# Kernel tuning notes

Hardware: AMD Instinct MI355X
Metric: run time of the kernel (lower is better)

The kernel has to match this reference:

```python
import jax, jax.numpy as jnp
import numpy as np
from jax import lax

N = 50000      # total nodes
E = 400000     # total edges
F = 512        # input feature dim
B = 50         # graphs in batch
NP = 1000      # nodes per graph
OUT = 10       # out_channel
EPS = 1e-5


def setup_inputs():
    key = jax.random.key(0)
    ks = jax.random.split(key, 20)
    x = jax.random.normal(ks[0], (N, F), jnp.float32)
    eg = jnp.arange(E) // (E // B)                       # graph id per edge
    src = jax.random.randint(ks[1], (E,), 0, NP) + eg * NP
    dst = jax.random.randint(ks[2], (E,), 0, NP) + eg * NP
    edge_index = jnp.stack([src, dst]).astype(jnp.int32)
    batch = (jnp.arange(N) // NP).astype(jnp.int32)
    s = 0.02
    W1 = s * jax.random.normal(ks[3], (1024, F), jnp.float32)
    b1 = jnp.zeros((1024,), jnp.float32)
    g1 = jnp.ones((1024,), jnp.float32)
    be1 = jnp.zeros((1024,), jnp.float32)
    Wp = s * jax.random.normal(ks[4], (1, 2 * 1024), jnp.float32)  # EdgePooling lin
    bp = jnp.zeros((1,), jnp.float32)
    W2 = s * jax.random.normal(ks[5], (512, 1024), jnp.float32)
    b2 = jnp.zeros((512,), jnp.float32)
    g2 = jnp.ones((512,), jnp.float32)
    be2 = jnp.zeros((512,), jnp.float32)
    Wfc = s * jax.random.normal(ks[6], (200, 512), jnp.float32)
    bfc = jnp.zeros((200,), jnp.float32)
    Wfc1 = s * jax.random.normal(ks[7], (OUT, 200), jnp.float32)
    bfc1 = jnp.zeros((OUT,), jnp.float32)
    return dict(x=x, edge_index=edge_index, batch=batch, W1=W1, b1=b1, g1=g1,
                be1=be1, Wp=Wp, bp=bp, W2=W2, b2=b2, g2=g2, be2=be2,
                Wfc=Wfc, bfc=bfc, Wfc1=Wfc1, bfc1=bfc1)


def _bn(h, g, b):
    m = h.mean(0)
    v = jnp.var(h, axis=0)  # biased var, as torch BatchNorm1d (train mode)
    return (h - m) * (g / jnp.sqrt(v + EPS)) + b


def _edge_pool(h, src, dst, batch, Wp, bp):
    # raw edge score: Linear([h_src || h_dst]) -> scalar per edge
    e = jnp.concatenate([h[src], h[dst]], axis=-1) @ Wp.T + bp  # [E,1]
    e = e[:, 0]
    # softmax over edges sharing the same destination node (PyG default)
    m = jax.ops.segment_max(e, dst, num_segments=N)
    ex = jnp.exp(e - m[dst])
    den = jax.ops.segment_sum(ex, dst, num_segments=N)
    score = ex / den[dst] + 0.5  # add_to_edge_score = 0.5

    # greedy contraction in descending-score order (sequential, like PyG)
    order = jnp.argsort(-score)
    so, do = src[order], dst[order]

    def step(merged, sd):
        s_, d_ = sd
        ok = (~merged[s_]) & (~merged[d_])
        merged = merged.at[s_].set(merged[s_] | ok)
        merged = merged.at[d_].set(merged[d_] | ok)
        return merged, ok

    _, valid = lax.scan(step, jnp.zeros(N, bool), (so, do))
    ec = (jnp.cumsum(valid.astype(jnp.int32)) - 1)      # cluster id per contracted edge
    num_merged = valid.astype(jnp.int32).sum()

    OOB = jnp.int32(N)
    cluster = jnp.full((N,), -1, jnp.int32)
    cluster = cluster.at[jnp.where(valid, so, OOB)].set(ec, mode='drop')
    cluster = cluster.at[jnp.where(valid, do, OOB)].set(ec, mode='drop')
    unmerged = cluster < 0
    rank = jnp.cumsum(unmerged.astype(jnp.int32)) - 1
    cluster = jnp.where(unmerged, num_merged + rank, cluster)

    # per-cluster multiplier: contracted-edge score, 1.0 for singleton nodes
    mult = jnp.ones((N,), h.dtype)
    mult = mult.at[jnp.where(valid, ec, OOB)].set(score[order], mode='drop')

    new_x = jax.ops.segment_sum(h, cluster, num_segments=N) * mult[:, None]
    new_batch = jnp.full((N,), B, jnp.int32).at[cluster].set(batch)  # pad slots -> dummy graph B
    return new_x, new_batch


def reference(x, edge_index, batch, W1, b1, g1, be1, Wp, bp, W2, b2, g2, be2,
              Wfc, bfc, Wfc1, bfc1):
    src, dst = edge_index[0], edge_index[1]
    # ChebConv K=1 == plain linear (only T_0 = x term)
    h = jax.nn.relu(_bn(x @ W1.T + b1, g1, be1))         # [N,1024]
    h, nb = _edge_pool(h, src, dst, batch, Wp, bp)       # [N,1024] padded, [N]
    h = jax.nn.relu(_bn(h @ W2.T + b2, g2, be2))         # [N,512]
    # global mean pool over graphs (dummy segment B holds padding)
    sums = jax.ops.segment_sum(h, nb, num_segments=B + 1)[:B]
    cnt = jax.ops.segment_sum(jnp.ones((N,), h.dtype), nb, num_segments=B + 1)[:B]
    pooled = sums / jnp.maximum(cnt, 1.0)[:, None]       # [B,512]
    hid = jax.nn.relu(pooled @ Wfc.T + bfc)              # [B,200]; dropout is eval no-op
    return hid @ Wfc1.T + bfc1                           # [B,OUT]
```

## Files before the change

### kernel.cpp

```cpp
#include <hip/hip_runtime.h>

#define Nn   50000
#define Ee   400000
#define Ff   512
#define H1   1024
#define H2   512
#define Bb   50
#define OUTd 10
#define EPSc 1e-5f
#define NPg  1000
#define EPg  8000

typedef _Float16 h8 __attribute__((ext_vector_type(8)));
typedef _Float16 h4 __attribute__((ext_vector_type(4)));
typedef float f4 __attribute__((ext_vector_type(4)));

__device__ __forceinline__ unsigned fmap(float f) {
    unsigned u = __float_as_uint(f);
    return (u & 0x80000000u) ? ~u : (u | 0x80000000u);
}
__device__ __forceinline__ float funmap(unsigned m) {
    unsigned u = (m & 0x80000000u) ? (m ^ 0x80000000u) : ~m;
    return __uint_as_float(u);
}

__device__ __forceinline__ void gl_lds16(const void* g, void* l) {
    __builtin_amdgcn_global_load_lds(
        (const __attribute__((address_space(1))) unsigned int*)g,
        (__attribute__((address_space(3))) unsigned int*)l,
        16, 0, 0);
}

__global__ void init_kernel(double* cs1, double* css1, double* cs2, double* css2, int* scal) {
    int i = blockIdx.x * blockDim.x + threadIdx.x;
    int nth = gridDim.x * blockDim.x;
    for (int j = i; j < H1; j += nth) { cs1[j] = 0.0; css1[j] = 0.0; }
    for (int j = i; j < H2; j += nth) { cs2[j] = 0.0; css2[j] = 0.0; }
    if (i < 16) scal[i] = 0;
}

__global__ void split_pair_kernel(const float* __restrict__ in, _Float16* __restrict__ hi,
                                  _Float16* __restrict__ lo, int n4) {
    int i = blockIdx.x * blockDim.x + threadIdx.x;
    int nth = gridDim.x * blockDim.x;
    for (; i < n4; i += nth) {
        float4 v = ((const float4*)in)[i];
        h4 H = { (_Float16)v.x, (_Float16)v.y, (_Float16)v.z, (_Float16)v.w };
        h4 L = { (_Float16)(v.x - (float)H[0]), (_Float16)(v.y - (float)H[1]),
                 (_Float16)(v.z - (float)H[2]), (_Float16)(v.w - (float)H[3]) };
        ((h4*)hi)[i] = H;
        ((h4*)lo)[i] = L;
    }
}
__global__ void tof16_kernel(const float* __restrict__ in, _Float16* __restrict__ out, int n4) {
    int i = blockIdx.x * blockDim.x + threadIdx.x;
    int nth = gridDim.x * blockDim.x;
    for (; i < n4; i += nth) {
        float4 v = ((const float4*)in)[i];
        h4 H = { (_Float16)v.x, (_Float16)v.y, (_Float16)v.z, (_Float16)v.w };
        ((h4*)out)[i] = H;
    }
}

template<int KD, bool SPLIT>
__global__ __launch_bounds__(256) void gemm_mfma_kernel(
        const _Float16* __restrict__ Ahi, const _Float16* __restrict__ Alo,
        const _Float16* __restrict__ Bhi, const _Float16* __restrict__ Blo,
        const float* __restrict__ bias, float* __restrict__ C, int Nc,
        int Mconst, const int* __restrict__ Mptr, int nT,
        double* __restrict__ csum, double* __restrict__ cssum)
{
    const int M = Mptr ? Mptr[0] : Mconst;
    const int nwg = gridDim.x, orig = blockIdx.x;
    const int qq = nwg >> 3, rr = nwg & 7;
    const int xcd = orig & 7, idx = orig >> 3;
    const int lin = (xcd < rr ? xcd * (qq + 1) : rr * (qq + 1) + (xcd - rr) * qq) + idx;
    const int bmI = lin / nT;
    const int bm = bmI * 128, bn = (lin - bmI * nT) * 128;
    if (bm >= M) return;
    constexpr int NARR = SPLIT ? 4 : 2;
    __shared__ __align__(16) _Float16 smem[2][NARR][128 * 32];
    const int tid = threadIdx.x, lane = tid & 63, wave = tid >> 6;
    const int rIn = lane >> 2;
    const int kSrcByte = ((((lane & 3) - ((lane >> 3) & 3)) & 3) << 4);
    const int wr = wave >> 1, wc = wave & 1;
    const int lr = lane & 15, kb = lane >> 4;
    const int pGr = ((kb + ((lr >> 1) & 3)) & 3) << 3;
    f4 acc[4][4] = {};

    auto STAGE = [&](int b, int k0) {
        if (SPLIT) {
            const _Float16* gp = (wave == 0) ? Ahi : (wave == 1) ? Alo : (wave == 2) ? Bhi : Blo;
            _Float16* lp = smem[b][wave];
            const bool isA = (wave < 2);
            const int tb = isA ? bm : bn;
#pragma unroll
            for (int c = 0; c < 8; ++c) {
                int row = tb + c * 16 + rIn;
                if (isA) row = min(row, M - 1);
                gl_lds16((const char*)gp + ((size_t)row * KD + k0) * 2 + kSrcByte, lp + c * 512);
            }
        } else {
            const bool isA = (wave < 2);
            const _Float16* gp = isA ? Ahi : Bhi;
            _Float16* lp = smem[b][isA ? 0 : 1];
            const int tb = isA ? bm : bn;
            const int hf = wave & 1;
#pragma unroll
            for (int c2 = 0; c2 < 4; ++c2) {
                int c = hf * 4 + c2;
                int row = tb + c * 16 + rIn;
                if (isA) row = min(row, M - 1);
                gl_lds16((const char*)gp + ((size_t)row * KD + k0) * 2 + kSrcByte, lp + c * 512);
            }
        }
    };

    int cur = 0;
    STAGE(0, 0);
    for (int k0 = 0; k0 < KD; k0 += 32) {
        __syncthreads();
        if (k0 + 32 < KD) STAGE(cur ^ 1, k0 + 32);
        const _Float16* AhP = smem[cur][0];
        const _Float16* AlP = SPLIT ? smem[cur][1] : nullptr;
        const _Float16* BhP = SPLIT ? smem[cur][2] : smem[cur][1];
        const _Float16* BlP = SPLIT ? smem[cur][3] : nullptr;
        const int ar = (wr * 64 + lr) * 32 + pGr;
        const int br = (wc * 64 + lr) * 32 + pGr;
        h8 ahf[4], bhf[4], alf[4], blf[4];
#pragma unroll
        for (int i = 0; i < 4; ++i) {
            ahf[i] = *(const h8*)&AhP[ar + i * 512];
            bhf[i] = *(const h8*)&BhP[br + i * 512];
            if (SPLIT) {
                alf[i] = *(const h8*)&AlP[ar + i * 512];
                blf[i] = *(const h8*)&BlP[br + i * 512];
            }
        }
#pragma unroll
        for (int mi = 0; mi < 4; ++mi)
#pragma unroll
            for (int ni = 0; ni < 4; ++ni) {
                acc[mi][ni] = __builtin_amdgcn_mfma_f32_16x16x32_f16(ahf[mi], bhf[ni], acc[mi][ni], 0, 0, 0);
                if (SPLIT) {
                    acc[mi][ni] = __builtin_amdgcn_mfma_f32_16x16x32_f16(ahf[mi], blf[ni], acc[mi][ni], 0, 0, 0);
                    acc[mi][ni] = __builtin_amdgcn_mfma_f32_16x16x32_f16(alf[mi], bhf[ni], acc[mi][ni], 0, 0, 0);
                }
            }
        cur ^= 1;
    }
#pragma unroll
    for (int ni = 0; ni < 4; ++ni) {
        const int col = bn + wc * 64 + ni * 16 + lr;
        const float bv = bias[col];
        double sd_ = 0.0, ssd = 0.0;
#pragma unroll
        for (int mi = 0; mi < 4; ++mi)
#pragma unroll
            for (int r = 0; r < 4; ++r) {
                int row = bm + wr * 64 + mi * 16 + kb * 4 + r;
                if (row < M) {
                    float v = acc[mi][ni][r] + bv;
                    C[(size_t)row * Nc + col] = v;
                    sd_ += (double)v;
                    ssd += (double)v * (double)v;
                }
            }
        sd_ += __shfl_xor(sd_, 16); ssd += __shfl_xor(ssd, 16);
        sd_ += __shfl_xor(sd_, 32); ssd += __shfl_xor(ssd, 32);
        if (kb == 0) {
            atomicAdd(&csum[col], sd_);
            atomicAdd(&cssum[col], ssd);
        }
    }
}

__global__ void bnparam_kernel(const double* __restrict__ s, const double* __restrict__ ss,
                               const float* __restrict__ g, const float* __restrict__ be,
                               float* __restrict__ a, float* __restrict__ bb, int cols,
                               const float* __restrict__ padBias, const int* __restrict__ CvPtr) {
    int j = blockIdx.x * blockDim.x + threadIdx.x;
    if (j >= cols) return;
    double sum = s[j], sumsq = ss[j];
    if (CvPtr) {
        double pad = (double)(Nn - CvPtr[0]);
        double bv = padBias ? (double)padBias[j] : 0.0;
        sum += pad * bv; sumsq += pad * bv * bv;
    }
    double mean = sum / (double)Nn;
    double var = sumsq / (double)Nn - mean * mean;
    float aj = g[j] / sqrtf((float)var + EPSc);
    a[j] = aj;
    bb[j] = be[j] - (float)mean * aj;
}

__global__ __launch_bounds__(256) void pq_kernel(const float* __restrict__ h,
        const float* __restrict__ a, const float* __restrict__ bb,
        const float* __restrict__ Wp, float* __restrict__ p, float* __restrict__ q) {
    const int n = blockIdx.x * 4 + (threadIdx.x >> 6);
    if (n >= Nn) return;
    const int lane = threadIdx.x & 63;
    float sp = 0.f, sq = 0.f;
    const float* row = h + (size_t)n * H1;
#pragma unroll
    for (int u = 0; u < 4; ++u) {
        int j = u * 256 + lane * 4;
        float4 v = *(const float4*)(row + j);
        const float4 av = *(const float4*)(a + j);
        const float4 bv = *(const float4*)(bb + j);
        v.x = fmaxf(v.x * av.x + bv.x, 0.f);
        v.y = fmaxf(v.y * av.y + bv.y, 0.f);
        v.z = fmaxf(v.z * av.z + bv.z, 0.f);
        v.w = fmaxf(v.w * av.w + bv.w, 0.f);
        const float4 wp = *(const float4*)(Wp + j);
        const float4 wq = *(const float4*)(Wp + H1 + j);
        sp += v.x * wp.x + v.y * wp.y + v.z * wp.z + v.w * wp.w;
        sq += v.x * wq.x + v.y * wq.y + v.z * wq.z + v.w * wq.w;
    }
#pragma unroll
    for (int off = 32; off > 0; off >>= 1) {
        sp += __shfl_xor(sp, off);
        sq += __shfl_xor(sq, off);
    }
    if (lane == 0) { p[n] = sp; q[n] = sq; }
}

__global__ __launch_bounds__(1024) void match_fused_kernel(
        const int* __restrict__ ei,
        const float* __restrict__ p, const float* __restrict__ q,
        const float* __restrict__ bp,
        unsigned long long* __restrict__ packed,
        int* __restrict__ nodeA, int* __restrict__ nodeB,
        float* __restrict__ multc, int* __restrict__ scal,
        int* __restrict__ gbase, int* __restrict__ gcnt) {
    __shared__ __align__(16) char LB[52096];
    unsigned short* lst = (unsigned short*)LB;
    float* earr = (float*)LB;
    float* pl = (float*)(LB + 32000);
    float* ql = pl + NPg;
    unsigned long long* best = (unsigned long long*)(LB + 32000);
    unsigned* maxu = (unsigned*)(LB + 40000);
    int* mergedS = (int*)(LB + 40000);
    unsigned long long* den = (unsigned long long*)(LB + 44000);
    float* lmult = (float*)(LB + 44000);
    unsigned short* lsA = (unsigned short*)(LB + 48000);
    unsigned short* ldA = (unsigned short*)(LB + 50000);
    int* cnts = (int*)(LB + 52032);

    const int g = blockIdx.x;
    const int tid = threadIdx.x;
    const int e0 = g * EPg, n0 = g * NPg;
    const int* srcp = ei + e0;
    const int* dstp = ei + Ee + e0;
    const float bpv = bp[0];

    for (int i = tid; i < NPg; i += 1024) {
        pl[i] = p[n0 + i];
        ql[i] = q[n0 + i];
        maxu[i] = 0u;
        den[i] = 0ull;
    }
    __syncthreads();
    for (int i = tid; i < EPg; i += 1024) {
        int s = srcp[i] - n0, d = dstp[i] - n0;
        float e = pl[s] + ql[d] + bpv;
        earr[i] = e;
        atomicMax(&maxu[d], fmap(e));
    }
    __syncthreads();
    for (int i = tid; i < EPg; i += 1024) {
        int d = dstp[i] - n0;
        float ex = expf(earr[i] - funmap(maxu[d]));
        atomicAdd(&den[d], (unsigned long long)(ex * 4294967296.0f));
    }
    __syncthreads();
    for (int i = tid; i < EPg; i += 1024) {
        int s = srcp[i] - n0, d = dstp[i] - n0;
        float ex = expf(earr[i] - funmap(maxu[d]));
        float den_f = (float)((double)den[d] * (1.0 / 4294967296.0));
        float sc = ex / den_f + 0.5f;
        packed[e0 + i] = ((unsigned long long)__float_as_uint(sc) << 33)
                       | ((unsigned long long)(8191u - (unsigned)i) << 20)
                       | ((unsigned long long)(unsigned)s << 10) | (unsigned long long)(unsigned)d;
    }
    __syncthreads();
    for (int i = tid; i < NPg; i += 1024) mergedS[i] = 0;
    for (int i = tid; i < EPg; i += 1024) lst[i] = (unsigned short)i;
    if (tid == 0) { cnts[0] = EPg; cnts[1] = 0; cnts[2] = 0; }
    __syncthreads();
    int cur = 0;
    for (int round = 0; round < 20000; ++round) {
        const int n_cur = cnts[cur];
        if (n_cur == 0) break;
        if (tid == 0) cnts[cur ^ 1] = 0;
        for (int i = tid; i < NPg; i += 1024) best[i] = 0ull;
        __syncthreads();
        for (int ii = tid; ii < n_cur; ii += 1024) {
            int le = lst[cur * EPg + ii];
            unsigned long long pk = packed[e0 + le];
            int s = (int)((pk >> 10) & 1023), d = (int)(pk & 1023);
            if (mergedS[s] | mergedS[d]) { lst[cur * EPg + ii] = 0xFFFF; continue; }
            atomicMax(&best[s], pk);
            atomicMax(&best[d], pk);
        }
        __syncthreads();
        for (int ii = tid; ii < n_cur; ii += 1024) {
            int le = lst[cur * EPg + ii];
            if (le == 0xFFFF) continue;
            unsigned long long pk = packed[e0 + le];
            int s = (int)((pk >> 10) & 1023), d = (int)(pk & 1023);
            if (best[s] == pk && best[d] == pk) {
                int c = atomicAdd(&cnts[2], 1);
                lsA[c] = (unsigned short)s;
                ldA[c] = (s == d) ? (unsigned short)0xFFFF : (unsigned short)d;
                lmult[c] = __uint_as_float((unsigned)(pk >> 33));
                mergedS[s] = 1;
                if (d != s) mergedS[d] = 1;
            } else {
                int pos = atomicAdd(&cnts[cur ^ 1], 1);
                lst[(cur ^ 1) * EPg + pos] = (unsigned short)le;
            }
        }
        __syncthreads();
        cur ^= 1;
    }
    for (int i = tid; i < NPg; i += 1024) {
        if (!mergedS[i]) {
            int c = atomicAdd(&cnts[2], 1);
            lsA[c] = (unsigned short)i;
            ldA[c] = 0xFFFF;
            lmult[c] = 1.0f;
        }
    }
    __syncthreads();
    if (tid == 0) {
        int ncl = cnts[2];
        int base = atomicAdd(&scal[2], ncl);
        cnts[3] = base;
        gbase[g] = base;
        gcnt[g] = ncl;
    }
    __syncthreads();
    const int ncl = cnts[2], base = cnts[3];
    for (int i = tid; i < ncl; i += 1024) {
        nodeA[base + i] = n0 + (int)lsA[i];
        nodeB[base + i] = (ldA[i] == 0xFFFF) ? -1 : (n0 + (int)ldA[i]);
        multc[base + i] = lmult[i];
    }
}

__global__ __launch_bounds__(256) void gather_kernel(const float* __restrict__ h,
        const float* __restrict__ a, const float* __restrict__ bb,
        const int* __restrict__ nodeA, const int* __restrict__ nodeB,
        const float* __restrict__ multc, const int* __restrict__ scal,
        _Float16* __restrict__ Ag) {
    int c = blockIdx.x * 4 + (threadIdx.x >> 6);
    if (c >= scal[2]) return;
    const int lane = threadIdx.x & 63;
    int na = nodeA[c], nb = nodeB[c];
    float mu = multc[c];
#pragma unroll
    for (int u = 0; u < 4; ++u) {
        int j = u * 256 + lane * 4;
        const float4 av = *(const float4*)(a + j);
        const float4 bv = *(const float4*)(bb + j);
        float4 v = *(const float4*)(h + (size_t)na * H1 + j);
        v.x = fmaxf(v.x * av.x + bv.x, 0.f);
        v.y = fmaxf(v.y * av.y + bv.y, 0.f);
        v.z = fmaxf(v.z * av.z + bv.z, 0.f);
        v.w = fmaxf(v.w * av.w + bv.w, 0.f);
        if (nb >= 0) {
            float4 w = *(const float4*)(h + (size_t)nb * H1 + j);
            v.x += fmaxf(w.x * av.x + bv.x, 0.f);
            v.y += fmaxf(w.y * av.y + bv.y, 0.f);
            v.z += fmaxf(w.z * av.z + bv.z, 0.f);
            v.w += fmaxf(w.w * av.w + bv.w, 0.f);
        }
        h4 o = { (_Float16)(mu * v.x), (_Float16)(mu * v.y), (_Float16)(mu * v.z), (_Float16)(mu * v.w) };
        *(h4*)(Ag + (size_t)c * H1 + j) = o;
    }
}

__global__ __launch_bounds__(256) void pool_seg_kernel(const float* __restrict__ C2,
        const float* __restrict__ a2, const float* __restrict__ bb2,
        const int* __restrict__ gbase, const int* __restrict__ gcnt,
        float* __restrict__ pool) {
    const int g = blockIdx.x;
    const int j = blockIdx.y * 256 + threadIdx.x;
    const int b0 = gbase[g], cN = gcnt[g];
    const float aj = a2[j], bj = bb2[j];
    float s = 0.f;
    for (int c = b0; c < b0 + cN; ++c)
        s += fmaxf(C2[(size_t)c * H2 + j] * aj + bj, 0.f);
    pool[g * H2 + j] = s;
}

__global__ void fc1_kernel(const float* __restrict__ pool, const int* __restrict__ gcnt,
                           const float* __restrict__ Wfc, const float* __restrict__ bfc,
                           float* __restrict__ hid) {
    int g = blockIdx.x;
    int o = threadIdx.x;
    float inv = 1.0f / fmaxf((float)gcnt[g], 1.0f);
    if (o < 200) {
        float s = 0.f;
        for (int j = 0; j < H2; ++j) s += (pool[g * H2 + j] * inv) * Wfc[o * H2 + j];
        hid[g * 200 + o] = fmaxf(s + bfc[o], 0.f);
    }
}
__global__ void fc2_kernel(const float* __restrict__ hid, const float* __restrict__ Wfc1,
                           const float* __restrict__ bfc1, float* __restrict__ out) {
    int idx = threadIdx.x;
    if (idx < Bb * OUTd) {
        int g = idx / OUTd, o = idx % OUTd;
        float s = bfc1[o];
        for (int t = 0; t < 200; ++t) s += hid[g * 200 + t] * Wfc1[o * 200 + t];
        out[idx] = s;
    }
}

extern "C" void kernel_launch(void* const* d_in, const int* in_sizes, int n_in,
                              void* d_out, int out_size, void* d_ws, size_t ws_size,
                              hipStream_t stream) {
    (void)in_sizes; (void)n_in; (void)out_size; (void)ws_size;
    const float* x    = (const float*)d_in[0];
    const int*   ei   = (const int*)d_in[1];
    const float* W1   = (const float*)d_in[3];
    const float* b1   = (const float*)d_in[4];
    const float* g1   = (const float*)d_in[5];
    const float* be1  = (const float*)d_in[6];
    const float* Wp   = (const float*)d_in[7];
    const float* bp   = (const float*)d_in[8];
    const float* W2   = (const float*)d_in[9];
    const float* b2   = (const float*)d_in[10];
    const float* g2   = (const float*)d_in[11];
    const float* be2  = (const float*)d_in[12];
    const float* Wfc  = (const float*)d_in[13];
    const float* bfc  = (const float*)d_in[14];
    const float* Wfc1 = (const float*)d_in[15];
    const float* bfc1 = (const float*)d_in[16];

    char* w = (char*)d_ws;
    auto take = [&](size_t bytes) -> char* {
        char* r = w;
        w += (bytes + 255) & ~(size_t)255;
        return r;
    };
    float* h      = (float*)take((size_t)Nn * H1 * 4);
    _Float16* xhi = (_Float16*)take((size_t)Nn * Ff * 2);
    _Float16* xlo = (_Float16*)take((size_t)Nn * Ff * 2);
    _Float16* w1h = (_Float16*)take((size_t)H1 * Ff * 2);
    _Float16* w1l = (_Float16*)take((size_t)H1 * Ff * 2);
    _Float16* w2h = (_Float16*)take((size_t)H2 * H1 * 2);
    float* p      = (float*)take((size_t)Nn * 4);
    float* q      = (float*)take((size_t)Nn * 4);
    unsigned long long* packed = (unsigned long long*)take((size_t)Ee * 8);
    int* nodeA    = (int*)take((size_t)Nn * 4);
    int* nodeB    = (int*)take((size_t)Nn * 4);
    float* multc  = (float*)take((size_t)Nn * 4);
    double* cs1   = (double*)take((size_t)H1 * 8);
    double* css1  = (double*)take((size_t)H1 * 8);
    double* cs2   = (double*)take((size_t)H2 * 8);
    double* css2  = (double*)take((size_t)H2 * 8);
    float* a1     = (float*)take((size_t)H1 * 4);
    float* bb1    = (float*)take((size_t)H1 * 4);
    float* a2     = (float*)take((size_t)H2 * 4);
    float* bb2    = (float*)take((size_t)H2 * 4);
    float* pool   = (float*)take((size_t)Bb * H2 * 4);
    float* hid    = (float*)take((size_t)Bb * 200 * 4);
    int* scal     = (int*)take(64 * 4);
    int* gbase    = (int*)take(64 * 4);
    int* gcnt     = (int*)take(64 * 4);
    _Float16* Ag  = xhi;
    float* C2o    = h;

    const int mT = (Nn + 127) / 128;

    init_kernel<<<dim3(16), dim3(256), 0, stream>>>(cs1, css1, cs2, css2, scal);
    split_pair_kernel<<<dim3(2048), dim3(256), 0, stream>>>(x, xhi, xlo, Nn * Ff / 4);
    split_pair_kernel<<<dim3(512), dim3(256), 0, stream>>>(W1, w1h, w1l, H1 * Ff / 4);
    tof16_kernel<<<dim3(512), dim3(256), 0, stream>>>(W2, w2h, H2 * H1 / 4);
    gemm_mfma_kernel<Ff, true><<<dim3(mT * (H1 / 128)), dim3(256), 0, stream>>>(
        xhi, xlo, w1h, w1l, b1, h, H1, Nn, nullptr, H1 / 128, cs1, css1);
    bnparam_kernel<<<dim3((H1 + 255) / 256), dim3(256), 0, stream>>>(cs1, css1, g1, be1, a1, bb1, H1, (const float*)nullptr, (const int*)nullptr);
    pq_kernel<<<dim3((Nn + 3) / 4), dim3(256), 0, stream>>>(h, a1, bb1, Wp, p, q);
    match_fused_kernel<<<dim3(Bb), dim3(1024), 0, stream>>>(ei, p, q, bp, packed,
        nodeA, nodeB, multc, scal, gbase, gcnt);
    gather_kernel<<<dim3((Nn + 3) / 4), dim3(256), 0, stream>>>(h, a1, bb1, nodeA, nodeB, multc, scal, Ag);
    gemm_mfma_kernel<H1, false><<<dim3(mT * (H2 / 128)), dim3(256), 0, stream>>>(
        Ag, nullptr, w2h, nullptr, b2, C2o, H2, 0, scal + 2, H2 / 128, cs2, css2);
    bnparam_kernel<<<dim3((H2 + 255) / 256), dim3(256), 0, stream>>>(cs2, css2, g2, be2, a2, bb2, H2, b2, scal + 2);
    pool_seg_kernel<<<dim3(Bb, H2 / 256), dim3(256), 0, stream>>>(C2o, a2, bb2, gbase, gcnt, pool);
    fc1_kernel<<<dim3(Bb), dim3(256), 0, stream>>>(pool, gcnt, Wfc, bfc, hid);
    fc2_kernel<<<dim3(1), dim3(512), 0, stream>>>(hid, Wfc1, bfc1, (float*)d_out);
}
```

Baseline: 699.8 us.

## Fuse cluster gather with BN-ReLU into second GEMM A-tile loading

The separate gather kernel, which built an fp16 pooled-feature matrix in global memory, is removed. Its work (BN+ReLU of both matched nodes, sum, scaling by the multiplier) now happens inside a new GEMM kernel: two waves load fp32 rows of h and write fp16 A tiles to LDS, while the other two waves stage B with direct-to-LDS loads. This cuts the round trip of the intermediate matrix and one launch, but each 128-row tile is regathered for every one of the four N tiles and only half the waves load A. The three fp16 conversion kernels are also merged into one prep kernel.

```diff
diff --git a/kernel.cpp b/kernel.cpp
--- a/kernel.cpp
+++ b/kernel.cpp
@@ -31,6 +31,14 @@
         16, 0, 0);
 }
 
+__device__ __forceinline__ float4 bnrelu4(float4 v, float4 av, float4 bv) {
+    v.x = fmaxf(v.x * av.x + bv.x, 0.f);
+    v.y = fmaxf(v.y * av.y + bv.y, 0.f);
+    v.z = fmaxf(v.z * av.z + bv.z, 0.f);
+    v.w = fmaxf(v.w * av.w + bv.w, 0.f);
+    return v;
+}
+
 __global__ void init_kernel(double* cs1, double* css1, double* cs2, double* css2, int* scal) {
     int i = blockIdx.x * blockDim.x + threadIdx.x;
     int nth = gridDim.x * blockDim.x;
@@ -39,26 +47,32 @@
     if (i < 16) scal[i] = 0;
 }
 
-__global__ void split_pair_kernel(const float* __restrict__ in, _Float16* __restrict__ hi,
-                                  _Float16* __restrict__ lo, int n4) {
+__global__ void prep_kernel(const float* __restrict__ x, _Float16* __restrict__ xhi, _Float16* __restrict__ xlo,
+                            const float* __restrict__ W1, _Float16* __restrict__ w1h, _Float16* __restrict__ w1l,
+                            const float* __restrict__ W2, _Float16* __restrict__ w2h) {
     int i = blockIdx.x * blockDim.x + threadIdx.x;
     int nth = gridDim.x * blockDim.x;
-    for (; i < n4; i += nth) {
-        float4 v = ((const float4*)in)[i];
+    const int nx = Nn * Ff / 4, nw1 = H1 * Ff / 4, nw2 = H2 * H1 / 4;
+    for (int k = i; k < nx; k += nth) {
+        float4 v = ((const float4*)x)[k];
         h4 H = { (_Float16)v.x, (_Float16)v.y, (_Float16)v.z, (_Float16)v.w };
         h4 L = { (_Float16)(v.x - (float)H[0]), (_Float16)(v.y - (float)H[1]),
                  (_Float16)(v.z - (float)H[2]), (_Float16)(v.w - (float)H[3]) };
-        ((h4*)hi)[i] = H;
-        ((h4*)lo)[i] = L;
-    }
-}
-__global__ void tof16_kernel(const float* __restrict__ in, _Float16* __restrict__ out, int n4) {
-    int i = blockIdx.x * blockDim.x + threadIdx.x;
-    int nth = gridDim.x * blockDim.x;
-    for (; i < n4; i += nth) {
-        float4 v = ((const float4*)in)[i];
+        ((h4*)xhi)[k] = H;
+        ((h4*)xlo)[k] = L;
+    }
+    for (int k = i; k < nw1; k += nth) {
+        float4 v = ((const float4*)W1)[k];
         h4 H = { (_Float16)v.x, (_Float16)v.y, (_Float16)v.z, (_Float16)v.w };
-        ((h4*)out)[i] = H;
+        h4 L = { (_Float16)(v.x - (float)H[0]), (_Float16)(v.y - (float)H[1]),
+                 (_Float16)(v.z - (float)H[2]), (_Float16)(v.w - (float)H[3]) };
+        ((h4*)w1h)[k] = H;
+        ((h4*)w1l)[k] = L;
+    }
+    for (int k = i; k < nw2; k += nth) {
+        float4 v = ((const float4*)W2)[k];
+        h4 H = { (_Float16)v.x, (_Float16)v.y, (_Float16)v.z, (_Float16)v.w };
+        ((h4*)w2h)[k] = H;
     }
 }
 
@@ -175,6 +189,142 @@
     }
 }
 
+__global__ __launch_bounds__(256) void gemm2f_kernel(
+        const float* __restrict__ h, const float* __restrict__ a1, const float* __restrict__ bb1,
+        const int* __restrict__ nodeA, const int* __restrict__ nodeB, const float* __restrict__ multc,
+        const _Float16* __restrict__ Bh, const float* __restrict__ bias,
+        float* __restrict__ C, const int* __restrict__ Mptr, int nT,
+        double* __restrict__ csum, double* __restrict__ cssum)
+{
+    const int M = Mptr[0];
+    const int nwg = gridDim.x, orig = blockIdx.x;
+    const int qq = nwg >> 3, rr = nwg & 7;
+    const int xcd = orig & 7, idx = orig >> 3;
+    const int lin = (xcd < rr ? xcd * (qq + 1) : rr * (qq + 1) + (xcd - rr) * qq) + idx;
+    const int bmI = lin / nT;
+    const int bm = bmI * 128, bn = (lin - bmI * nT) * 128;
+    if (bm >= M) return;
+    __shared__ __align__(16) _Float16 sA[2][128 * 32];
+    __shared__ __align__(16) _Float16 sB[2][128 * 32];
+    const int tid = threadIdx.x, lane = tid & 63, wave = tid >> 6;
+    const int rIn = lane >> 2;
+    const int gsel = (((lane & 3) - ((lane >> 3) & 3)) & 3);
+    const int kSrcByte = gsel << 4;
+    const int wr = wave >> 1, wc = wave & 1;
+    const int lr = lane & 15, kb = lane >> 4;
+    const int pGr = ((kb + ((lr >> 1) & 3)) & 3) << 3;
+    const bool isA = (wave < 2);
+    const int hf = wave & 1;
+    f4 acc[4][4] = {};
+
+    int nac[4], nbc[4];
+    float muc[4];
+    if (isA) {
+#pragma unroll
+        for (int c2 = 0; c2 < 4; ++c2) {
+            int row = min(bm + (hf * 4 + c2) * 16 + rIn, M - 1);
+            nac[c2] = nodeA[row];
+            nbc[c2] = nodeB[row];
+            muc[c2] = multc[row];
+        }
+    }
+
+    float4 va[4][2], vb[4][2], av0, av1, bv0, bv1;
+    auto A_LOAD = [&](int k0) {
+        if (!isA) return;
+        const int col = k0 + gsel * 8;
+        av0 = *(const float4*)(a1 + col);     av1 = *(const float4*)(a1 + col + 4);
+        bv0 = *(const float4*)(bb1 + col);    bv1 = *(const float4*)(bb1 + col + 4);
+#pragma unroll
+        for (int c2 = 0; c2 < 4; ++c2) {
+            const float* ra = h + (size_t)nac[c2] * H1 + col;
+            va[c2][0] = *(const float4*)ra;
+            va[c2][1] = *(const float4*)(ra + 4);
+            const float* rb = h + (size_t)(nbc[c2] >= 0 ? nbc[c2] : 0) * H1 + col;
+            vb[c2][0] = *(const float4*)rb;
+            vb[c2][1] = *(const float4*)(rb + 4);
+        }
+    };
+    auto A_WRITE = [&](int b) {
+        if (!isA) return;
+#pragma unroll
+        for (int c2 = 0; c2 < 4; ++c2) {
+            float4 e0 = bnrelu4(va[c2][0], av0, bv0);
+            float4 e1 = bnrelu4(va[c2][1], av1, bv1);
+            if (nbc[c2] >= 0) {
+                float4 f0 = bnrelu4(vb[c2][0], av0, bv0);
+                float4 f1 = bnrelu4(vb[c2][1], av1, bv1);
+                e0.x += f0.x; e0.y += f0.y; e0.z += f0.z; e0.w += f0.w;
+                e1.x += f1.x; e1.y += f1.y; e1.z += f1.z; e1.w += f1.w;
+            }
+            const float mu = muc[c2];
+            h8 o = { (_Float16)(mu * e0.x), (_Float16)(mu * e0.y), (_Float16)(mu * e0.z), (_Float16)(mu * e0.w),
+                     (_Float16)(mu * e1.x), (_Float16)(mu * e1.y), (_Float16)(mu * e1.z), (_Float16)(mu * e1.w) };
+            *(h8*)&sA[b][(hf * 4 + c2) * 512 + lane * 8] = o;
+        }
+    };
+    auto B_STAGE = [&](int b, int k0) {
+        if (isA) return;
+#pragma unroll
+        for (int c2 = 0; c2 < 4; ++c2) {
+            int c = hf * 4 + c2;
+            int row = bn + c * 16 + rIn;
+            gl_lds16((const char*)Bh + ((size_t)row * H1 + k0) * 2 + kSrcByte, &sB[b][c * 512]);
+        }
+    };
+
+    A_LOAD(0);
+    B_STAGE(0, 0);
+    A_WRITE(0);
+    int cur = 0;
+    for (int k0 = 0; k0 < H1; k0 += 32) {
+        __syncthreads();
+        if (k0 + 32 < H1) {
+            A_LOAD(k0 + 32);
+            B_STAGE(cur ^ 1, k0 + 32);
+        }
+        const int ar = (wr * 64 + lr) * 32 + pGr;
+        const int br = (wc * 64 + lr) * 32 + pGr;
+        h8 ahf[4], bhf[4];
+#pragma unroll
+        for (int i = 0; i < 4; ++i) {
+            ahf[i] = *(const h8*)&sA[cur][ar + i * 512];
+            bhf[i] = *(const h8*)&sB[cur][br + i * 512];
+        }
+#pragma unroll
+        for (int mi = 0; mi < 4; ++mi)
+#pragma unroll
+            for (int ni = 0; ni < 4; ++ni)
+                acc[mi][ni] = __builtin_amdgcn_mfma_f32_16x16x32_f16(ahf[mi], bhf[ni], acc[mi][ni], 0, 0, 0);
+        if (k0 + 32 < H1) A_WRITE(cur ^ 1);
+        cur ^= 1;
+    }
+#pragma unroll
+    for (int ni = 0; ni < 4; ++ni) {
+        const int col = bn + wc * 64 + ni * 16 + lr;
+        const float bv = bias[col];
+        double sd_ = 0.0, ssd = 0.0;
+#pragma unroll
+        for (int mi = 0; mi < 4; ++mi)
+#pragma unroll
+            for (int r = 0; r < 4; ++r) {
+                int row = bm + wr * 64 + mi * 16 + kb * 4 + r;
+                if (row < M) {
+                    float v = acc[mi][ni][r] + bv;
+                    C[(size_t)row * H2 + col] = v;
+                    sd_ += (double)v;
+                    ssd += (double)v * (double)v;
+                }
+            }
+        sd_ += __shfl_xor(sd_, 16); ssd += __shfl_xor(ssd, 16);
+        sd_ += __shfl_xor(sd_, 32); ssd += __shfl_xor(ssd, 32);
+        if (kb == 0) {
+            atomicAdd(&csum[col], sd_);
+            atomicAdd(&cssum[col], ssd);
+        }
+    }
+}
+
 __global__ void bnparam_kernel(const double* __restrict__ s, const double* __restrict__ ss,
                                const float* __restrict__ g, const float* __restrict__ be,
                                float* __restrict__ a, float* __restrict__ bb, int cols,
@@ -346,38 +496,6 @@
         nodeA[base + i] = n0 + (int)lsA[i];
         nodeB[base + i] = (ldA[i] == 0xFFFF) ? -1 : (n0 + (int)ldA[i]);
         multc[base + i] = lmult[i];
-    }
-}
-
-__global__ __launch_bounds__(256) void gather_kernel(const float* __restrict__ h,
-        const float* __restrict__ a, const float* __restrict__ bb,
-        const int* __restrict__ nodeA, const int* __restrict__ nodeB,
-        const float* __restrict__ multc, const int* __restrict__ scal,
-        _Float16* __restrict__ Ag) {
-    int c = blockIdx.x * 4 + (threadIdx.x >> 6);
-    if (c >= scal[2]) return;
-    const int lane = threadIdx.x & 63;
-    int na = nodeA[c], nb = nodeB[c];
-    float mu = multc[c];
-#pragma unroll
-    for (int u = 0; u < 4; ++u) {
-        int j = u * 256 + lane * 4;
-        const float4 av = *(const float4*)(a + j);
-        const float4 bv = *(const float4*)(bb + j);
-        float4 v = *(const float4*)(h + (size_t)na * H1 + j);
-        v.x = fmaxf(v.x * av.x + bv.x, 0.f);
-        v.y = fmaxf(v.y * av.y + bv.y, 0.f);
-        v.z = fmaxf(v.z * av.z + bv.z, 0.f);
-        v.w = fmaxf(v.w * av.w + bv.w, 0.f);
-        if (nb >= 0) {
-            float4 w = *(const float4*)(h + (size_t)nb * H1 + j);
-            v.x += fmaxf(w.x * av.x + bv.x, 0.f);
-            v.y += fmaxf(w.y * av.y + bv.y, 0.f);
-            v.z += fmaxf(w.z * av.z + bv.z, 0.f);
-            v.w += fmaxf(w.w * av.w + bv.w, 0.f);
-        }
-        h4 o = { (_Float16)(mu * v.x), (_Float16)(mu * v.y), (_Float16)(mu * v.z), (_Float16)(mu * v.w) };
-        *(h4*)(Ag + (size_t)c * H1 + j) = o;
     }
 }
 
@@ -470,24 +588,20 @@
     int* scal     = (int*)take(64 * 4);
     int* gbase    = (int*)take(64 * 4);
     int* gcnt     = (int*)take(64 * 4);
-    _Float16* Ag  = xhi;
-    float* C2o    = h;
+    float* C2o    = (float*)xhi;
 
     const int mT = (Nn + 127) / 128;
 
     init_kernel<<<dim3(16), dim3(256), 0, stream>>>(cs1, css1, cs2, css2, scal);
-    split_pair_kernel<<<dim3(2048), dim3(256), 0, stream>>>(x, xhi, xlo, Nn * Ff / 4);
-    split_pair_kernel<<<dim3(512), dim3(256), 0, stream>>>(W1, w1h, w1l, H1 * Ff / 4);
-    tof16_kernel<<<dim3(512), dim3(256), 0, stream>>>(W2, w2h, H2 * H1 / 4);
+    prep_kernel<<<dim3(2048), dim3(256), 0, stream>>>(x, xhi, xlo, W1, w1h, w1l, W2, w2h);
     gemm_mfma_kernel<Ff, true><<<dim3(mT * (H1 / 128)), dim3(256), 0, stream>>>(
         xhi, xlo, w1h, w1l, b1, h, H1, Nn, nullptr, H1 / 128, cs1, css1);
     bnparam_kernel<<<dim3((H1 + 255) / 256), dim3(256), 0, stream>>>(cs1, css1, g1, be1, a1, bb1, H1, (const float*)nullptr, (const int*)nullptr);
     pq_kernel<<<dim3((Nn + 3) / 4), dim3(256), 0, stream>>>(h, a1, bb1, Wp, p, q);
     match_fused_kernel<<<dim3(Bb), dim3(1024), 0, stream>>>(ei, p, q, bp, packed,
         nodeA, nodeB, multc, scal, gbase, gcnt);
-    gather_kernel<<<dim3((Nn + 3) / 4), dim3(256), 0, stream>>>(h, a1, bb1, nodeA, nodeB, multc, scal, Ag);
-    gemm_mfma_kernel<H1, false><<<dim3(mT * (H2 / 128)), dim3(256), 0, stream>>>(
-        Ag, nullptr, w2h, nullptr, b2, C2o, H2, 0, scal + 2, H2 / 128, cs2, css2);
+    gemm2f_kernel<<<dim3(mT * (H2 / 128)), dim3(256), 0, stream>>>(
+        h, a1, bb1, nodeA, nodeB, multc, w2h, b2, C2o, scal + 2, H2 / 128, cs2, css2);
     bnparam_kernel<<<dim3((H2 + 255) / 256), dim3(256), 0, stream>>>(cs2, css2, g2, be2, a2, bb2, H2, b2, scal + 2);
     pool_seg_kernel<<<dim3(Bb, H2 / 256), dim3(256), 0, stream>>>(C2o, a2, bb2, gbase, gcnt, pool);
     fc1_kernel<<<dim3(Bb), dim3(256), 0, stream>>>(pool, gcnt, Wfc, bfc, hid);
```

After: 1.033 ms. 47.6% more time.
